# Kernel optimization log

Hardware: AMD Instinct MI355X
Metric: run time of the kernel (lower is better)

## Reference

```python
import jax, jax.numpy as jnp
import numpy as np

H = 16        # num_heads
D_HEAD = 128  # head_dim
D = H * D_HEAD  # hidden_size = 2048


def setup_inputs() -> dict:
    key = jax.random.key(0)
    ks = jax.random.split(key, 9)
    s = 1.0 / np.sqrt(D)
    x = jax.random.normal(ks[0], (2, 2048, D), dtype=jnp.float32)
    Wq = jax.random.uniform(ks[1], (D, D), jnp.float32, -s, s)
    bq = jax.random.uniform(ks[2], (D,), jnp.float32, -s, s)
    Wk = jax.random.uniform(ks[3], (D, D), jnp.float32, -s, s)
    bk = jax.random.uniform(ks[4], (D,), jnp.float32, -s, s)
    Wv = jax.random.uniform(ks[5], (D, D), jnp.float32, -s, s)
    bv = jax.random.uniform(ks[6], (D,), jnp.float32, -s, s)
    Wo = jax.random.uniform(ks[7], (D, D), jnp.float32, -s, s)
    bo = jax.random.uniform(ks[8], (D,), jnp.float32, -s, s)
    return {"x": x, "Wq": Wq, "bq": bq, "Wk": Wk, "bk": bk,
            "Wv": Wv, "bv": bv, "Wo": Wo, "bo": bo}


def reference(x, Wq, bq, Wk, bk, Wv, bv, Wo, bo):
    B, T, _ = x.shape
    # Linear projections (torch Linear: x @ W.T + b)
    Q = x @ Wq.T + bq
    K = x @ Wk.T + bk
    V = x @ Wv.T + bv
    # [B, T, H, Dh] -> [B, H, T, Dh]
    Q = Q.reshape(B, T, H, D_HEAD).transpose(0, 2, 1, 3)
    K = K.reshape(B, T, H, D_HEAD).transpose(0, 2, 1, 3)
    V = V.reshape(B, T, H, D_HEAD).transpose(0, 2, 1, 3)
    scores = jnp.einsum('bhqd,bhkd->bhqk', Q, K) / jnp.sqrt(jnp.float32(D_HEAD))
    causal = jnp.tril(jnp.ones((T, T), dtype=bool))
    scores = jnp.where(causal, scores, -jnp.inf)
    probs = jax.nn.softmax(scores, axis=-1)
    ctx = jnp.einsum('bhqk,bhkd->bhqd', probs, V)  # [B, H, T, Dh]
    merged = ctx.transpose(0, 2, 1, 3).reshape(B, T, D)
    return merged @ Wo.T + bo
```

## Files before the change

kernel.cpp:

```cpp
#include <hip/hip_runtime.h>
#include <hip/hip_bf16.h>
#include <math.h>

typedef unsigned short ushort_t;
typedef short bf16x8 __attribute__((ext_vector_type(8)));
typedef float f32x4 __attribute__((ext_vector_type(4)));
typedef float f32x16 __attribute__((ext_vector_type(16)));

#define NH 16
#define DH 128
#define DM 2048
#define TSEQ 2048
#define BT 4096

__device__ __forceinline__ void async16(const void* g, void* l) {
  __builtin_amdgcn_global_load_lds(
      (const __attribute__((address_space(1))) void*)g,
      (__attribute__((address_space(3))) void*)l, 16, 0, 0);
}

__device__ __forceinline__ f32x4 mfma16(bf16x8 a, bf16x8 b, f32x4 c) {
  return __builtin_amdgcn_mfma_f32_16x16x32_bf16(a, b, c, 0, 0, 0);
}
__device__ __forceinline__ f32x16 mfma32(bf16x8 a, bf16x8 b, f32x16 c) {
  return __builtin_amdgcn_mfma_f32_32x32x16_bf16(a, b, c, 0, 0, 0);
}

__device__ __forceinline__ ushort_t f2bf(float f) {
  __hip_bfloat16 h = __float2bfloat16(f);
  return *reinterpret_cast<ushort_t*>(&h);
}
__device__ __forceinline__ unsigned cvtpk_bf16(float lo, float hi_) {
  unsigned r;
  asm("v_cvt_pk_bf16_f32 %0, %1, %2" : "=v"(r) : "v"(lo), "v"(hi_));
  return r;
}
__device__ __forceinline__ float fexp2(float x) {
  float r; asm("v_exp_f32 %0, %1" : "=v"(r) : "v"(x)); return r;
}

__global__ void cvt_all_kernel(const float* __restrict__ x,
                               const float* __restrict__ Wq, const float* __restrict__ Wk,
                               const float* __restrict__ Wv, const float* __restrict__ Wo,
                               ushort_t* __restrict__ xb,
                               ushort_t* __restrict__ Wqb, ushort_t* __restrict__ Wkb,
                               ushort_t* __restrict__ Wvb, ushort_t* __restrict__ Wob)
{
  const int i = blockIdx.x * blockDim.x + threadIdx.x;
  const float* src; ushort_t* dst; int off;
  if (i < (1 << 21)) {
    src = x; dst = xb; off = i;
  } else {
    const int j = i - (1 << 21);
    const int w = j >> 20;
    off = j & ((1 << 20) - 1);
    src = (w == 0) ? Wq : (w == 1) ? Wk : (w == 2) ? Wv : Wo;
    dst = (w == 0) ? Wqb : (w == 1) ? Wkb : (w == 2) ? Wvb : Wob;
  }
  const float4 v = reinterpret_cast<const float4*>(src)[off];
  ushort4 u;
  u.x = f2bf(v.x); u.y = f2bf(v.y); u.z = f2bf(v.z); u.w = f2bf(v.w);
  reinterpret_cast<ushort4*>(dst)[off] = u;
}

__device__ __forceinline__ void stage_ab(const ushort_t* __restrict__ A,
                                         const ushort_t* __restrict__ Wp,
                                         int m0, int n0, int k0,
                                         ushort_t* AsB, ushort_t* BsB,
                                         int w, int l)
{
#pragma unroll
  for (int i = 0; i < 4; ++i) {
    const int rb = (i * 4 + w) * 8;
    const int r = rb + (l >> 3);
    const int c = ((l & 7) * 8) ^ ((r & 7) * 8);
    async16(A  + (size_t)(m0 + r) * DM + k0 + c, AsB + rb * 64);
    async16(Wp + (size_t)(n0 + r) * DM + k0 + c, BsB + rb * 64);
  }
}

template<int MODE>
__global__ __launch_bounds__(256)
void gemm_kernel(const ushort_t* __restrict__ A,
                 const ushort_t* __restrict__ W_0, const ushort_t* __restrict__ W_1,
                 const ushort_t* __restrict__ W_2,
                 const float* __restrict__ b_0, const float* __restrict__ b_1,
                 const float* __restrict__ b_2,
                 ushort_t* __restrict__ outQ, ushort_t* __restrict__ outK,
                 ushort_t* __restrict__ outVt, float* __restrict__ outF)
{
  constexpr int NK = DM / 64;
  __shared__ __attribute__((aligned(16))) ushort_t As[2][128 * 64];
  __shared__ __attribute__((aligned(16))) ushort_t Bs[2][128 * 64];

  const int z = (MODE == 0) ? blockIdx.z : 0;
  const ushort_t* Wp = (MODE == 0) ? (z == 0 ? W_0 : (z == 1 ? W_1 : W_2)) : W_0;
  const float* bias  = (MODE == 0) ? (z == 0 ? b_0 : (z == 1 ? b_1 : b_2)) : b_0;

  const int n0 = blockIdx.x * 128;
  const int m0 = blockIdx.y * 128;
  const int tid = threadIdx.x;
  const int w = tid >> 6, l = tid & 63;
  const int wm = w >> 1, wn = w & 1;
  const int l15 = l & 15, l4 = l >> 4;

  f32x4 zero = {0.f, 0.f, 0.f, 0.f};
  f32x4 acc[4][4];
#pragma unroll
  for (int i = 0; i < 4; ++i)
#pragma unroll
    for (int j = 0; j < 4; ++j) acc[i][j] = zero;

  stage_ab(A, Wp, m0, n0, 0, As[0], Bs[0], w, l);

  for (int kt = 0; kt < NK; ++kt) {
    const int cur = kt & 1;
    if (kt + 1 < NK) {
      stage_ab(A, Wp, m0, n0, (kt + 1) * 64, As[cur ^ 1], Bs[cur ^ 1], w, l);
      asm volatile("s_waitcnt vmcnt(8)" ::: "memory");
    } else {
      asm volatile("s_waitcnt vmcnt(0)" ::: "memory");
    }
    __builtin_amdgcn_s_barrier();

#pragma unroll
    for (int ks = 0; ks < 2; ++ks) {
      bf16x8 af[4], bfr[4];
#pragma unroll
      for (int mf = 0; mf < 4; ++mf) {
        const int row = wm * 64 + mf * 16 + l15;
        const int byte_ = row * 128 + ((l4 * 16 + ks * 64) ^ ((row & 7) << 4));
        af[mf] = *reinterpret_cast<const bf16x8*>(reinterpret_cast<const char*>(As[cur]) + byte_);
      }
#pragma unroll
      for (int nf = 0; nf < 4; ++nf) {
        const int row = wn * 64 + nf * 16 + l15;
        const int byte_ = row * 128 + ((l4 * 16 + ks * 64) ^ ((row & 7) << 4));
        bfr[nf] = *reinterpret_cast<const bf16x8*>(reinterpret_cast<const char*>(Bs[cur]) + byte_);
      }
      __builtin_amdgcn_s_setprio(1);
#pragma unroll
      for (int mf = 0; mf < 4; ++mf)
#pragma unroll
        for (int nf = 0; nf < 4; ++nf)
          acc[mf][nf] = mfma16(af[mf], bfr[nf], acc[mf][nf]);
      __builtin_amdgcn_s_setprio(0);
    }
    asm volatile("" ::: "memory");
    __builtin_amdgcn_s_barrier();
  }

#pragma unroll
  for (int nf = 0; nf < 4; ++nf) {
    const int n = n0 + wn * 64 + nf * 16 + l15;
    const float bv = bias[n];
#pragma unroll
    for (int mf = 0; mf < 4; ++mf) {
#pragma unroll
      for (int r = 0; r < 4; ++r) {
        const int m = m0 + wm * 64 + mf * 16 + l4 * 4 + r;
        const float v = acc[mf][nf][r] + bv;
        if (MODE == 1) {
          outF[(size_t)m * DM + n] = v;
        } else {
          const int b = m >> 11, t = m & 2047;
          const int hh = n >> 7, d = n & 127;
          const ushort_t val = f2bf(v);
          if (z == 2) {
            outVt[((size_t)(b * NH + hh) * DH + d) * TSEQ + t] = val;
          } else {
            ushort_t* dst = (z == 0) ? outQ : outK;
            dst[((size_t)(b * NH + hh) * TSEQ + t) * DH + d] = val;
          }
        }
      }
    }
  }
}

__device__ __forceinline__ void stage_kv(const ushort_t* __restrict__ Kg,
                                         const ushort_t* __restrict__ Vt,
                                         size_t kbase, size_t vbase, int kv0,
                                         ushort_t* KsB, ushort_t* VsB, int tid)
{
#pragma unroll
  for (int i = 0; i < 4; ++i) {
    const int idx = i * 256 + tid;
    const int r = idx >> 4, ch = idx & 15;
    const int c = (ch ^ (r & 7)) * 8;
    async16(Kg + kbase + (size_t)(kv0 + r) * DH + c, KsB + idx * 8);
  }
#pragma unroll
  for (int i = 0; i < 4; ++i) {
    const int idx = i * 256 + tid;
    const int d = idx >> 3, ch = idx & 7;
    const int c = (ch ^ (d & 7)) * 8;
    async16(Vt + vbase + (size_t)d * TSEQ + kv0 + c, VsB + idx * 8);
  }
}

__global__ __launch_bounds__(256)
void attn_kernel(const ushort_t* __restrict__ Q, const ushort_t* __restrict__ Kg,
                 const ushort_t* __restrict__ Vt, ushort_t* __restrict__ ctx)
{
  __shared__ __attribute__((aligned(16))) ushort_t Ks[2][64 * 128];
  __shared__ __attribute__((aligned(16))) ushort_t Vs[2][128 * 64];

  const int fid = (int)blockIdx.x + 16 * (int)blockIdx.y;
  const int xcd = fid & 7;
  const int s   = fid >> 3;
  const int bh  = xcd * 4 + (s & 3);
  const int qt  = (s < 32) ? (15 - (s >> 2)) : ((s - 32) >> 2);

  const int tid = threadIdx.x, w = tid >> 6, l = tid & 63;
  const int l31 = l & 31, hi = l >> 5;
  const size_t kbase = (size_t)bh * TSEQ * DH;
  const size_t vbase = (size_t)bh * DH * TSEQ;
  const int bq0 = qt * 128;
  const int wq0 = bq0 + w * 32;
  const int NT = qt * 2 + 2;
  const int q = wq0 + l31;
  const float C2 = 0.12753842f;
  const float NEG = -3.0e38f;

  bf16x8 aq[8];
  {
    const ushort_t* qp = Q + kbase + (size_t)q * DH + hi * 8;
#pragma unroll
    for (int st = 0; st < 8; ++st)
      aq[st] = *reinterpret_cast<const bf16x8*>(qp + st * 16);
  }

  f32x16 o[4] = {};
  float m_r = NEG, l_r = 0.f;

  stage_kv(Kg, Vt, kbase, vbase, 0, Ks[0], Vs[0], tid);

  for (int kt = 0; kt < NT; ++kt) {
    const int kv0 = kt * 64, cur = kt & 1;
    if (kt + 1 < NT) {
      stage_kv(Kg, Vt, kbase, vbase, kv0 + 64, Ks[cur ^ 1], Vs[cur ^ 1], tid);
      asm volatile("s_waitcnt vmcnt(8)" ::: "memory");
    } else {
      asm volatile("s_waitcnt vmcnt(0)" ::: "memory");
    }
    __builtin_amdgcn_s_barrier();

    if (kv0 <= wq0 + 31) {
      const char* ksb = reinterpret_cast<const char*>(Ks[cur]);
      f32x16 s0 = {}, s1 = {};
      __builtin_amdgcn_s_setprio(1);
#pragma unroll
      for (int st = 0; st < 8; ++st) {
        const int byt = l31 * 256 + ((hi * 16 + st * 32) ^ ((l31 & 7) << 4));
        bf16x8 ak0 = *reinterpret_cast<const bf16x8*>(ksb + byt);
        bf16x8 ak1 = *reinterpret_cast<const bf16x8*>(ksb + byt + 8192);
        s0 = mfma32(ak0, aq[st], s0);
        s1 = mfma32(ak1, aq[st], s1);
      }
      __builtin_amdgcn_s_setprio(0);

      if (kv0 + 63 > wq0) {
#pragma unroll
        for (int r = 0; r < 16; ++r) {
          const int kvl = kv0 + (r & 3) + 8 * (r >> 2) + 4 * hi;
          if (kvl > q)      s0[r] = NEG;
          if (kvl + 32 > q) s1[r] = NEG;
        }
      }

      float t8[8];
#pragma unroll
      for (int r = 0; r < 8; ++r)
        t8[r] = fmaxf(fmaxf(s0[r], s0[r + 8]), fmaxf(s1[r], s1[r + 8]));
#pragma unroll
      for (int r = 0; r < 4; ++r) t8[r] = fmaxf(t8[r], t8[r + 4]);
      float mt = fmaxf(fmaxf(t8[0], t8[1]), fmaxf(t8[2], t8[3]));
      mt = fmaxf(mt, __shfl_xor(mt, 32));

      const float mnew = fmaxf(m_r, mt);
      if (!__all(mt <= m_r + 16.0f)) {
        const float alpha = fexp2((m_r - mnew) * C2);
        l_r *= alpha;
#pragma unroll
        for (int d0 = 0; d0 < 4; ++d0) o[d0] *= alpha;
        m_r = mnew;
      }

#pragma unroll
      for (int r = 0; r < 16; ++r) {
        s0[r] = fexp2((s0[r] - m_r) * C2);
        s1[r] = fexp2((s1[r] - m_r) * C2);
      }
      float sm[8];
#pragma unroll
      for (int r = 0; r < 8; ++r) sm[r] = (s0[r] + s0[r + 8]) + (s1[r] + s1[r + 8]);
#pragma unroll
      for (int r = 0; r < 4; ++r) sm[r] += sm[r + 4];
      float ls = (sm[0] + sm[1]) + (sm[2] + sm[3]);
      ls += __shfl_xor(ls, 32);
      l_r += ls;

      const char* vsb = reinterpret_cast<const char*>(Vs[cur]);
#pragma unroll
      for (int ks = 0; ks < 4; ++ks) {
        float pj[8];
#pragma unroll
        for (int j = 0; j < 8; ++j)
          pj[j] = (ks >> 1) ? s1[(ks & 1) * 8 + j] : s0[(ks & 1) * 8 + j];
        unsigned cA = cvtpk_bf16(pj[0], pj[1]);
        unsigned cB = cvtpk_bf16(pj[2], pj[3]);
        unsigned cC = cvtpk_bf16(pj[4], pj[5]);
        unsigned cD = cvtpk_bf16(pj[6], pj[7]);
        asm volatile("v_permlane32_swap_b32 %0, %1" : "+v"(cA), "+v"(cC));
        asm volatile("v_permlane32_swap_b32 %0, %1" : "+v"(cB), "+v"(cD));
        union { unsigned u[4]; bf16x8 v; } pa;
        pa.u[0] = cA; pa.u[1] = cB; pa.u[2] = cC; pa.u[3] = cD;
        __builtin_amdgcn_s_setprio(1);
#pragma unroll
        for (int d0 = 0; d0 < 4; ++d0) {
          const int byt = (d0 * 32 + l31) * 128 + ((ks * 32 + hi * 16) ^ ((l31 & 7) << 4));
          bf16x8 av = *reinterpret_cast<const bf16x8*>(vsb + byt);
          o[d0] = mfma32(av, pa.v, o[d0]);
        }
        __builtin_amdgcn_s_setprio(0);
      }
    }
    asm volatile("" ::: "memory");
    __builtin_amdgcn_s_barrier();
  }

  const size_t obase = (size_t)(bh >> 4) * TSEQ * DM + (size_t)(bh & 15) * DH;
  const float inv = 1.0f / l_r;
  ushort_t* cp = ctx + obase + (size_t)q * DM + hi * 4;
#pragma unroll
  for (int d0 = 0; d0 < 4; ++d0) {
#pragma unroll
    for (int g = 0; g < 4; ++g) {
      ushort4 u;
      u.x = f2bf(o[d0][4 * g + 0] * inv);
      u.y = f2bf(o[d0][4 * g + 1] * inv);
      u.z = f2bf(o[d0][4 * g + 2] * inv);
      u.w = f2bf(o[d0][4 * g + 3] * inv);
      *reinterpret_cast<ushort4*>(cp + d0 * 32 + 8 * g) = u;
    }
  }
}

extern "C" void kernel_launch(void* const* d_in, const int* in_sizes, int n_in,
                              void* d_out, int out_size, void* d_ws, size_t ws_size,
                              hipStream_t stream) {
  const float* x  = (const float*)d_in[0];
  const float* Wq = (const float*)d_in[1];
  const float* bq = (const float*)d_in[2];
  const float* Wk = (const float*)d_in[3];
  const float* bk = (const float*)d_in[4];
  const float* Wv = (const float*)d_in[5];
  const float* bv = (const float*)d_in[6];
  const float* Wo = (const float*)d_in[7];
  const float* bo = (const float*)d_in[8];
  float* out = (float*)d_out;

  char* ws = (char*)d_ws;
  ushort_t* xb  = (ushort_t*)ws;  ws += (size_t)BT * DM * 2;
  ushort_t* Wqb = (ushort_t*)ws;  ws += (size_t)DM * DM * 2;
  ushort_t* Wkb = (ushort_t*)ws;  ws += (size_t)DM * DM * 2;
  ushort_t* Wvb = (ushort_t*)ws;  ws += (size_t)DM * DM * 2;
  ushort_t* Wob = (ushort_t*)ws;  ws += (size_t)DM * DM * 2;
  ushort_t* Qb  = (ushort_t*)ws;  ws += (size_t)BT * DM * 2;
  ushort_t* Kb  = (ushort_t*)ws;  ws += (size_t)BT * DM * 2;
  ushort_t* Vtb = (ushort_t*)ws;  ws += (size_t)BT * DM * 2;
  ushort_t* ctxb = xb;

  cvt_all_kernel<<<6 * (1 << 20) / 256, 256, 0, stream>>>(
      x, Wq, Wk, Wv, Wo, xb, Wqb, Wkb, Wvb, Wob);

  gemm_kernel<0><<<dim3(16, 32, 3), 256, 0, stream>>>(
      xb, Wqb, Wkb, Wvb, bq, bk, bv, Qb, Kb, Vtb, nullptr);

  attn_kernel<<<dim3(TSEQ / 128, 32), 256, 0, stream>>>(Qb, Kb, Vtb, ctxb);

  gemm_kernel<1><<<dim3(16, 32, 1), 256, 0, stream>>>(
      ctxb, Wob, nullptr, nullptr, bo, nullptr, nullptr,
      nullptr, nullptr, nullptr, out);
}
```

Baseline: 278.5 us.

## Use 256x256-tile, 8-wave GEMM with quarter-staged pipeline for QKV projection

Replaces the 128x128 QKV projection GEMM with a new 512-thread kernel that computes a 256x256 output tile per block. The block loads A and B in 128-row halves and interleaves the four quadrant MFMA passes with async global-to-LDS staging of the next k-tile. The aim is more data reuse per byte loaded and better overlap of loads with MFMA work. The grid shrinks to 384 blocks with one block per CU, which risks an uneven tail and more barriers per k-step. The output projection is split into its own non-templated kernel with unchanged logic.

```diff
diff --git a/kernel.cpp b/kernel.cpp
--- a/kernel.cpp
+++ b/kernel.cpp
@@ -63,6 +63,148 @@
   reinterpret_cast<ushort4*>(dst)[off] = u;
 }
 
+__device__ __forceinline__ void stage_half_g(const ushort_t* __restrict__ src,
+                                             int row0, int k0,
+                                             ushort_t* dst, int tid) {
+#pragma unroll
+  for (int i = 0; i < 2; ++i) {
+    const int idx = i * 512 + tid;
+    const int r = idx >> 3, ch = idx & 7;
+    const int c = (ch ^ (r & 7)) * 8;
+    async16(src + (size_t)(row0 + r) * DM + k0 + c, dst + idx * 8);
+  }
+}
+
+__global__ __launch_bounds__(512, 1)
+void gemm256_kernel(const ushort_t* __restrict__ A,
+                    const ushort_t* __restrict__ W_0, const ushort_t* __restrict__ W_1,
+                    const ushort_t* __restrict__ W_2,
+                    const float* __restrict__ b_0, const float* __restrict__ b_1,
+                    const float* __restrict__ b_2,
+                    ushort_t* __restrict__ outQ, ushort_t* __restrict__ outK,
+                    ushort_t* __restrict__ outVt)
+{
+  constexpr int NK = DM / 64;
+  __shared__ __attribute__((aligned(16))) ushort_t As[2][2][128 * 64];
+  __shared__ __attribute__((aligned(16))) ushort_t Bs[2][2][128 * 64];
+
+  const int z = blockIdx.z;
+  const ushort_t* Wp = (z == 0 ? W_0 : (z == 1 ? W_1 : W_2));
+  const float* bias  = (z == 0 ? b_0 : (z == 1 ? b_1 : b_2));
+
+  const int n0 = blockIdx.x * 256;
+  const int m0 = blockIdx.y * 256;
+
+  const int tid = threadIdx.x;
+  const int w = tid >> 6, l = tid & 63;
+  const int wr = w >> 2, wc = w & 3;
+  const int l15 = l & 15, l4 = l >> 4;
+
+  f32x4 acc[2][2][4][2] = {};
+  bf16x8 afr[4][2], blo[2][2], bhi[2][2];
+
+#define LOAD_A(BUF, AH)                                                           \
+  { const char* p_ = reinterpret_cast<const char*>(As[BUF][AH]);                  \
+    _Pragma("unroll") for (int mf = 0; mf < 4; ++mf) {                            \
+      const int row_ = wr * 64 + mf * 16 + l15;                                   \
+      _Pragma("unroll") for (int ks = 0; ks < 2; ++ks)                            \
+        afr[mf][ks] = *reinterpret_cast<const bf16x8*>(                           \
+            p_ + row_ * 128 + ((l4 * 16 + ks * 64) ^ ((row_ & 7) << 4))); } }
+
+#define LOAD_B(BUF, BH, ARR)                                                      \
+  { const char* p_ = reinterpret_cast<const char*>(Bs[BUF][BH]);                  \
+    _Pragma("unroll") for (int nf = 0; nf < 2; ++nf) {                            \
+      const int row_ = wc * 32 + nf * 16 + l15;                                   \
+      _Pragma("unroll") for (int ks = 0; ks < 2; ++ks)                            \
+        ARR[nf][ks] = *reinterpret_cast<const bf16x8*>(                           \
+            p_ + row_ * 128 + ((l4 * 16 + ks * 64) ^ ((row_ & 7) << 4))); } }
+
+#define MMQ(AH, BH, ARR)                                                          \
+  __builtin_amdgcn_s_setprio(1);                                                  \
+  _Pragma("unroll") for (int mf = 0; mf < 4; ++mf)                                \
+  _Pragma("unroll") for (int nf = 0; nf < 2; ++nf)                                \
+  _Pragma("unroll") for (int ks = 0; ks < 2; ++ks)                                \
+    acc[AH][BH][mf][nf] = mfma16(afr[mf][ks], ARR[nf][ks], acc[AH][BH][mf][nf]);  \
+  __builtin_amdgcn_s_setprio(0);                                                  \
+  asm volatile("" ::: "memory");
+
+#define BAR() { asm volatile("" ::: "memory"); __builtin_amdgcn_s_barrier(); \
+                asm volatile("" ::: "memory"); }
+#define VMC(N) asm volatile("s_waitcnt vmcnt(" #N ")" ::: "memory")
+
+  stage_half_g(A,  m0,       0, As[0][0], tid);
+  stage_half_g(Wp, n0,       0, Bs[0][0], tid);
+  stage_half_g(Wp, n0 + 128, 0, Bs[0][1], tid);
+  stage_half_g(A,  m0 + 128, 0, As[0][1], tid);
+  VMC(4);
+  BAR();
+
+  for (int kt = 0; kt < NK; ++kt) {
+    const int buf = kt & 1, nb = buf ^ 1;
+    const int k1 = (kt + 1) * 64;
+    const bool more = (kt + 1 < NK);
+
+    LOAD_A(buf, 0); LOAD_B(buf, 0, blo);
+    if (more) stage_half_g(A, m0, k1, As[nb][0], tid);
+    BAR();
+    MMQ(0, 0, blo);
+    if (more) { VMC(4); } else { VMC(2); }
+    BAR();
+
+    LOAD_B(buf, 1, bhi);
+    if (more) stage_half_g(Wp, n0, k1, Bs[nb][0], tid);
+    BAR();
+    MMQ(0, 1, bhi);
+    if (more) { VMC(4); } else { VMC(0); }
+    BAR();
+
+    LOAD_A(buf, 1);
+    if (more) stage_half_g(Wp, n0 + 128, k1, Bs[nb][1], tid);
+    BAR();
+    MMQ(1, 1, bhi);
+    BAR();
+
+    if (more) stage_half_g(A, m0 + 128, k1, As[nb][1], tid);
+    BAR();
+    MMQ(1, 0, blo);
+    if (more) { VMC(4); }
+    BAR();
+  }
+
+#undef LOAD_A
+#undef LOAD_B
+#undef MMQ
+#undef BAR
+#undef VMC
+
+#pragma unroll
+  for (int Ah = 0; Ah < 2; ++Ah)
+#pragma unroll
+  for (int Bh = 0; Bh < 2; ++Bh)
+#pragma unroll
+  for (int nf = 0; nf < 2; ++nf) {
+    const int n = n0 + Bh * 128 + wc * 32 + nf * 16 + l15;
+    const float bv = bias[n];
+#pragma unroll
+    for (int mf = 0; mf < 4; ++mf) {
+#pragma unroll
+      for (int r = 0; r < 4; ++r) {
+        const int m = m0 + Ah * 128 + wr * 64 + mf * 16 + l4 * 4 + r;
+        const float v = acc[Ah][Bh][mf][nf][r] + bv;
+        const int b = m >> 11, t = m & 2047;
+        const int hh = n >> 7, d = n & 127;
+        const ushort_t val = f2bf(v);
+        if (z == 2) {
+          outVt[((size_t)(b * NH + hh) * DH + d) * TSEQ + t] = val;
+        } else {
+          ushort_t* dst = (z == 0) ? outQ : outK;
+          dst[((size_t)(b * NH + hh) * TSEQ + t) * DH + d] = val;
+        }
+      }
+    }
+  }
+}
+
 __device__ __forceinline__ void stage_ab(const ushort_t* __restrict__ A,
                                          const ushort_t* __restrict__ Wp,
                                          int m0, int n0, int k0,
@@ -79,23 +221,13 @@
   }
 }
 
-template<int MODE>
 __global__ __launch_bounds__(256)
-void gemm_kernel(const ushort_t* __restrict__ A,
-                 const ushort_t* __restrict__ W_0, const ushort_t* __restrict__ W_1,
-                 const ushort_t* __restrict__ W_2,
-                 const float* __restrict__ b_0, const float* __restrict__ b_1,
-                 const float* __restrict__ b_2,
-                 ushort_t* __restrict__ outQ, ushort_t* __restrict__ outK,
-                 ushort_t* __restrict__ outVt, float* __restrict__ outF)
+void gemm_proj_kernel(const ushort_t* __restrict__ A, const ushort_t* __restrict__ W_0,
+                      const float* __restrict__ b_0, float* __restrict__ outF)
 {
   constexpr int NK = DM / 64;
   __shared__ __attribute__((aligned(16))) ushort_t As[2][128 * 64];
   __shared__ __attribute__((aligned(16))) ushort_t Bs[2][128 * 64];
-
-  const int z = (MODE == 0) ? blockIdx.z : 0;
-  const ushort_t* Wp = (MODE == 0) ? (z == 0 ? W_0 : (z == 1 ? W_1 : W_2)) : W_0;
-  const float* bias  = (MODE == 0) ? (z == 0 ? b_0 : (z == 1 ? b_1 : b_2)) : b_0;
 
   const int n0 = blockIdx.x * 128;
   const int m0 = blockIdx.y * 128;
@@ -111,12 +243,12 @@
 #pragma unroll
     for (int j = 0; j < 4; ++j) acc[i][j] = zero;
 
-  stage_ab(A, Wp, m0, n0, 0, As[0], Bs[0], w, l);
+  stage_ab(A, W_0, m0, n0, 0, As[0], Bs[0], w, l);
 
   for (int kt = 0; kt < NK; ++kt) {
     const int cur = kt & 1;
     if (kt + 1 < NK) {
-      stage_ab(A, Wp, m0, n0, (kt + 1) * 64, As[cur ^ 1], Bs[cur ^ 1], w, l);
+      stage_ab(A, W_0, m0, n0, (kt + 1) * 64, As[cur ^ 1], Bs[cur ^ 1], w, l);
       asm volatile("s_waitcnt vmcnt(8)" ::: "memory");
     } else {
       asm volatile("s_waitcnt vmcnt(0)" ::: "memory");
@@ -153,26 +285,13 @@
 #pragma unroll
   for (int nf = 0; nf < 4; ++nf) {
     const int n = n0 + wn * 64 + nf * 16 + l15;
-    const float bv = bias[n];
+    const float bv = b_0[n];
 #pragma unroll
     for (int mf = 0; mf < 4; ++mf) {
 #pragma unroll
       for (int r = 0; r < 4; ++r) {
         const int m = m0 + wm * 64 + mf * 16 + l4 * 4 + r;
-        const float v = acc[mf][nf][r] + bv;
-        if (MODE == 1) {
-          outF[(size_t)m * DM + n] = v;
-        } else {
-          const int b = m >> 11, t = m & 2047;
-          const int hh = n >> 7, d = n & 127;
-          const ushort_t val = f2bf(v);
-          if (z == 2) {
-            outVt[((size_t)(b * NH + hh) * DH + d) * TSEQ + t] = val;
-          } else {
-            ushort_t* dst = (z == 0) ? outQ : outK;
-            dst[((size_t)(b * NH + hh) * TSEQ + t) * DH + d] = val;
-          }
-        }
+        outF[(size_t)m * DM + n] = acc[mf][nf][r] + bv;
       }
     }
   }
@@ -375,12 +494,10 @@
   cvt_all_kernel<<<6 * (1 << 20) / 256, 256, 0, stream>>>(
       x, Wq, Wk, Wv, Wo, xb, Wqb, Wkb, Wvb, Wob);
 
-  gemm_kernel<0><<<dim3(16, 32, 3), 256, 0, stream>>>(
-      xb, Wqb, Wkb, Wvb, bq, bk, bv, Qb, Kb, Vtb, nullptr);
+  gemm256_kernel<<<dim3(8, 16, 3), 512, 0, stream>>>(
+      xb, Wqb, Wkb, Wvb, bq, bk, bv, Qb, Kb, Vtb);
 
   attn_kernel<<<dim3(TSEQ / 128, 32), 256, 0, stream>>>(Qb, Kb, Vtb, ctxb);
 
-  gemm_kernel<1><<<dim3(16, 32, 1), 256, 0, stream>>>(
-      ctxb, Wob, nullptr, nullptr, bo, nullptr, nullptr,
-      nullptr, nullptr, nullptr, out);
-}
+  gemm_proj_kernel<<<dim3(16, 32), 256, 0, stream>>>(ctxb, Wob, bo, out);
+}
```

New measurement: 307.5 us. +10.4%, slower.

## Fuse Q/K/V projections into one GEMM kernel sharing the staged input tile

Applied to the files above, without the earlier changes.

Replaces the per-projection QKV GEMM launch (grid z=3) with a single 512-thread kernel. Each block stages its activation tile once and multiplies it against the matching Wq, Wk and Wv tiles, writing all three bf16 outputs. The aim is to stop reloading the activation tile three times. In exchange each block needs about 128KB of LDS and more accumulators per wave, which likely leaves one block per CU and a smaller grid. The output projection is split out into its own non-templated kernel with unchanged logic.

```diff
diff --git a/kernel.cpp b/kernel.cpp
--- a/kernel.cpp
+++ b/kernel.cpp
@@ -63,87 +63,90 @@
   reinterpret_cast<ushort4*>(dst)[off] = u;
 }
 
-__device__ __forceinline__ void stage_ab(const ushort_t* __restrict__ A,
-                                         const ushort_t* __restrict__ Wp,
-                                         int m0, int n0, int k0,
-                                         ushort_t* AsB, ushort_t* BsB,
-                                         int w, int l)
-{
-#pragma unroll
-  for (int i = 0; i < 4; ++i) {
-    const int rb = (i * 4 + w) * 8;
-    const int r = rb + (l >> 3);
-    const int c = ((l & 7) * 8) ^ ((r & 7) * 8);
-    async16(A  + (size_t)(m0 + r) * DM + k0 + c, AsB + rb * 64);
-    async16(Wp + (size_t)(n0 + r) * DM + k0 + c, BsB + rb * 64);
-  }
-}
-
-template<int MODE>
-__global__ __launch_bounds__(256)
-void gemm_kernel(const ushort_t* __restrict__ A,
-                 const ushort_t* __restrict__ W_0, const ushort_t* __restrict__ W_1,
-                 const ushort_t* __restrict__ W_2,
-                 const float* __restrict__ b_0, const float* __restrict__ b_1,
-                 const float* __restrict__ b_2,
-                 ushort_t* __restrict__ outQ, ushort_t* __restrict__ outK,
-                 ushort_t* __restrict__ outVt, float* __restrict__ outF)
+__device__ __forceinline__ void stage_half_g(const ushort_t* __restrict__ src,
+                                             int row0, int k0,
+                                             ushort_t* dst, int tid) {
+#pragma unroll
+  for (int i = 0; i < 2; ++i) {
+    const int idx = i * 512 + tid;
+    const int r = idx >> 3, ch = idx & 7;
+    const int c = (ch ^ (r & 7)) * 8;
+    async16(src + (size_t)(row0 + r) * DM + k0 + c, dst + idx * 8);
+  }
+}
+
+__global__ __launch_bounds__(512, 2)
+void gemm_qkv_fused(const ushort_t* __restrict__ A,
+                    const ushort_t* __restrict__ W_0, const ushort_t* __restrict__ W_1,
+                    const ushort_t* __restrict__ W_2,
+                    const float* __restrict__ b_0, const float* __restrict__ b_1,
+                    const float* __restrict__ b_2,
+                    ushort_t* __restrict__ outQ, ushort_t* __restrict__ outK,
+                    ushort_t* __restrict__ outVt)
 {
   constexpr int NK = DM / 64;
   __shared__ __attribute__((aligned(16))) ushort_t As[2][128 * 64];
-  __shared__ __attribute__((aligned(16))) ushort_t Bs[2][128 * 64];
-
-  const int z = (MODE == 0) ? blockIdx.z : 0;
-  const ushort_t* Wp = (MODE == 0) ? (z == 0 ? W_0 : (z == 1 ? W_1 : W_2)) : W_0;
-  const float* bias  = (MODE == 0) ? (z == 0 ? b_0 : (z == 1 ? b_1 : b_2)) : b_0;
+  __shared__ __attribute__((aligned(16))) ushort_t Bs[2][3][128 * 64];
 
   const int n0 = blockIdx.x * 128;
   const int m0 = blockIdx.y * 128;
   const int tid = threadIdx.x;
   const int w = tid >> 6, l = tid & 63;
-  const int wm = w >> 1, wn = w & 1;
+  const int wr = w >> 2, wc = w & 3;
   const int l15 = l & 15, l4 = l >> 4;
 
-  f32x4 zero = {0.f, 0.f, 0.f, 0.f};
-  f32x4 acc[4][4];
-#pragma unroll
-  for (int i = 0; i < 4; ++i)
-#pragma unroll
-    for (int j = 0; j < 4; ++j) acc[i][j] = zero;
-
-  stage_ab(A, Wp, m0, n0, 0, As[0], Bs[0], w, l);
+  f32x4 acc[3][4][2] = {};
+  bf16x8 afr[4][2], bfr[2][2];
+
+  stage_half_g(A,   m0, 0, As[0],    tid);
+  stage_half_g(W_0, n0, 0, Bs[0][0], tid);
+  stage_half_g(W_1, n0, 0, Bs[0][1], tid);
+  stage_half_g(W_2, n0, 0, Bs[0][2], tid);
 
   for (int kt = 0; kt < NK; ++kt) {
     const int cur = kt & 1;
     if (kt + 1 < NK) {
-      stage_ab(A, Wp, m0, n0, (kt + 1) * 64, As[cur ^ 1], Bs[cur ^ 1], w, l);
+      const int k1 = (kt + 1) * 64;
+      stage_half_g(A,   m0, k1, As[cur ^ 1],    tid);
+      stage_half_g(W_0, n0, k1, Bs[cur ^ 1][0], tid);
+      stage_half_g(W_1, n0, k1, Bs[cur ^ 1][1], tid);
+      stage_half_g(W_2, n0, k1, Bs[cur ^ 1][2], tid);
       asm volatile("s_waitcnt vmcnt(8)" ::: "memory");
     } else {
       asm volatile("s_waitcnt vmcnt(0)" ::: "memory");
     }
     __builtin_amdgcn_s_barrier();
 
-#pragma unroll
-    for (int ks = 0; ks < 2; ++ks) {
-      bf16x8 af[4], bfr[4];
+    {
+      const char* p_ = reinterpret_cast<const char*>(As[cur]);
 #pragma unroll
       for (int mf = 0; mf < 4; ++mf) {
-        const int row = wm * 64 + mf * 16 + l15;
-        const int byte_ = row * 128 + ((l4 * 16 + ks * 64) ^ ((row & 7) << 4));
-        af[mf] = *reinterpret_cast<const bf16x8*>(reinterpret_cast<const char*>(As[cur]) + byte_);
-      }
-#pragma unroll
-      for (int nf = 0; nf < 4; ++nf) {
-        const int row = wn * 64 + nf * 16 + l15;
-        const int byte_ = row * 128 + ((l4 * 16 + ks * 64) ^ ((row & 7) << 4));
-        bfr[nf] = *reinterpret_cast<const bf16x8*>(reinterpret_cast<const char*>(Bs[cur]) + byte_);
+        const int row_ = wr * 64 + mf * 16 + l15;
+#pragma unroll
+        for (int ks = 0; ks < 2; ++ks)
+          afr[mf][ks] = *reinterpret_cast<const bf16x8*>(
+              p_ + row_ * 128 + ((l4 * 16 + ks * 64) ^ ((row_ & 7) << 4)));
+      }
+    }
+#pragma unroll
+    for (int z = 0; z < 3; ++z) {
+      const char* p_ = reinterpret_cast<const char*>(Bs[cur][z]);
+#pragma unroll
+      for (int nf = 0; nf < 2; ++nf) {
+        const int row_ = wc * 32 + nf * 16 + l15;
+#pragma unroll
+        for (int ks = 0; ks < 2; ++ks)
+          bfr[nf][ks] = *reinterpret_cast<const bf16x8*>(
+              p_ + row_ * 128 + ((l4 * 16 + ks * 64) ^ ((row_ & 7) << 4)));
       }
       __builtin_amdgcn_s_setprio(1);
 #pragma unroll
       for (int mf = 0; mf < 4; ++mf)
 #pragma unroll
-        for (int nf = 0; nf < 4; ++nf)
-          acc[mf][nf] = mfma16(af[mf], bfr[nf], acc[mf][nf]);
+        for (int nf = 0; nf < 2; ++nf)
+#pragma unroll
+          for (int ks = 0; ks < 2; ++ks)
+            acc[z][mf][nf] = mfma16(afr[mf][ks], bfr[nf][ks], acc[z][mf][nf]);
       __builtin_amdgcn_s_setprio(0);
     }
     asm volatile("" ::: "memory");
@@ -151,20 +154,20 @@
   }
 
 #pragma unroll
-  for (int nf = 0; nf < 4; ++nf) {
-    const int n = n0 + wn * 64 + nf * 16 + l15;
-    const float bv = bias[n];
-#pragma unroll
-    for (int mf = 0; mf < 4; ++mf) {
-#pragma unroll
-      for (int r = 0; r < 4; ++r) {
-        const int m = m0 + wm * 64 + mf * 16 + l4 * 4 + r;
-        const float v = acc[mf][nf][r] + bv;
-        if (MODE == 1) {
-          outF[(size_t)m * DM + n] = v;
-        } else {
+  for (int z = 0; z < 3; ++z) {
+    const float* bias = (z == 0) ? b_0 : (z == 1) ? b_1 : b_2;
+#pragma unroll
+    for (int nf = 0; nf < 2; ++nf) {
+      const int n = n0 + wc * 32 + nf * 16 + l15;
+      const float bv = bias[n];
+      const int hh = n >> 7, d = n & 127;
+#pragma unroll
+      for (int mf = 0; mf < 4; ++mf) {
+#pragma unroll
+        for (int r = 0; r < 4; ++r) {
+          const int m = m0 + wr * 64 + mf * 16 + l4 * 4 + r;
+          const float v = acc[z][mf][nf][r] + bv;
           const int b = m >> 11, t = m & 2047;
-          const int hh = n >> 7, d = n & 127;
           const ushort_t val = f2bf(v);
           if (z == 2) {
             outVt[((size_t)(b * NH + hh) * DH + d) * TSEQ + t] = val;
@@ -173,6 +176,98 @@
             dst[((size_t)(b * NH + hh) * TSEQ + t) * DH + d] = val;
           }
         }
+      }
+    }
+  }
+}
+
+__device__ __forceinline__ void stage_ab(const ushort_t* __restrict__ A,
+                                         const ushort_t* __restrict__ Wp,
+                                         int m0, int n0, int k0,
+                                         ushort_t* AsB, ushort_t* BsB,
+                                         int w, int l)
+{
+#pragma unroll
+  for (int i = 0; i < 4; ++i) {
+    const int rb = (i * 4 + w) * 8;
+    const int r = rb + (l >> 3);
+    const int c = ((l & 7) * 8) ^ ((r & 7) * 8);
+    async16(A  + (size_t)(m0 + r) * DM + k0 + c, AsB + rb * 64);
+    async16(Wp + (size_t)(n0 + r) * DM + k0 + c, BsB + rb * 64);
+  }
+}
+
+__global__ __launch_bounds__(256)
+void gemm_proj_kernel(const ushort_t* __restrict__ A, const ushort_t* __restrict__ W_0,
+                      const float* __restrict__ b_0, float* __restrict__ outF)
+{
+  constexpr int NK = DM / 64;
+  __shared__ __attribute__((aligned(16))) ushort_t As[2][128 * 64];
+  __shared__ __attribute__((aligned(16))) ushort_t Bs[2][128 * 64];
+
+  const int n0 = blockIdx.x * 128;
+  const int m0 = blockIdx.y * 128;
+  const int tid = threadIdx.x;
+  const int w = tid >> 6, l = tid & 63;
+  const int wm = w >> 1, wn = w & 1;
+  const int l15 = l & 15, l4 = l >> 4;
+
+  f32x4 zero = {0.f, 0.f, 0.f, 0.f};
+  f32x4 acc[4][4];
+#pragma unroll
+  for (int i = 0; i < 4; ++i)
+#pragma unroll
+    for (int j = 0; j < 4; ++j) acc[i][j] = zero;
+
+  stage_ab(A, W_0, m0, n0, 0, As[0], Bs[0], w, l);
+
+  for (int kt = 0; kt < NK; ++kt) {
+    const int cur = kt & 1;
+    if (kt + 1 < NK) {
+      stage_ab(A, W_0, m0, n0, (kt + 1) * 64, As[cur ^ 1], Bs[cur ^ 1], w, l);
+      asm volatile("s_waitcnt vmcnt(8)" ::: "memory");
+    } else {
+      asm volatile("s_waitcnt vmcnt(0)" ::: "memory");
+    }
+    __builtin_amdgcn_s_barrier();
+
+#pragma unroll
+    for (int ks = 0; ks < 2; ++ks) {
+      bf16x8 af[4], bfr[4];
+#pragma unroll
+      for (int mf = 0; mf < 4; ++mf) {
+        const int row = wm * 64 + mf * 16 + l15;
+        const int byte_ = row * 128 + ((l4 * 16 + ks * 64) ^ ((row & 7) << 4));
+        af[mf] = *reinterpret_cast<const bf16x8*>(reinterpret_cast<const char*>(As[cur]) + byte_);
+      }
+#pragma unroll
+      for (int nf = 0; nf < 4; ++nf) {
+        const int row = wn * 64 + nf * 16 + l15;
+        const int byte_ = row * 128 + ((l4 * 16 + ks * 64) ^ ((row & 7) << 4));
+        bfr[nf] = *reinterpret_cast<const bf16x8*>(reinterpret_cast<const char*>(Bs[cur]) + byte_);
+      }
+      __builtin_amdgcn_s_setprio(1);
+#pragma unroll
+      for (int mf = 0; mf < 4; ++mf)
+#pragma unroll
+        for (int nf = 0; nf < 4; ++nf)
+          acc[mf][nf] = mfma16(af[mf], bfr[nf], acc[mf][nf]);
+      __builtin_amdgcn_s_setprio(0);
+    }
+    asm volatile("" ::: "memory");
+    __builtin_amdgcn_s_barrier();
+  }
+
+#pragma unroll
+  for (int nf = 0; nf < 4; ++nf) {
+    const int n = n0 + wn * 64 + nf * 16 + l15;
+    const float bv = b_0[n];
+#pragma unroll
+    for (int mf = 0; mf < 4; ++mf) {
+#pragma unroll
+      for (int r = 0; r < 4; ++r) {
+        const int m = m0 + wm * 64 + mf * 16 + l4 * 4 + r;
+        outF[(size_t)m * DM + n] = acc[mf][nf][r] + bv;
       }
     }
   }
@@ -375,12 +470,10 @@
   cvt_all_kernel<<<6 * (1 << 20) / 256, 256, 0, stream>>>(
       x, Wq, Wk, Wv, Wo, xb, Wqb, Wkb, Wvb, Wob);
 
-  gemm_kernel<0><<<dim3(16, 32, 3), 256, 0, stream>>>(
-      xb, Wqb, Wkb, Wvb, bq, bk, bv, Qb, Kb, Vtb, nullptr);
+  gemm_qkv_fused<<<dim3(16, 32), 512, 0, stream>>>(
+      xb, Wqb, Wkb, Wvb, bq, bk, bv, Qb, Kb, Vtb);
 
   attn_kernel<<<dim3(TSEQ / 128, 32), 256, 0, stream>>>(Qb, Kb, Vtb, ctxb);
 
-  gemm_kernel<1><<<dim3(16, 32, 1), 256, 0, stream>>>(
-      ctxb, Wob, nullptr, nullptr, bo, nullptr, nullptr,
-      nullptr, nullptr, nullptr, out);
-}
+  gemm_proj_kernel<<<dim3(16, 32), 256, 0, stream>>>(ctxb, Wob, bo, out);
+}
```

Result: faster. 271.9 us (-2.4%).
